# Optimization experiments

Hardware: AMD Instinct MI355X
Metric: run time of the kernel (lower is better)

Reference implementation:

```python
import jax, jax.numpy as jnp
import numpy as np

N_NODES = 100000
HID = 32
NUM_FEAT = 64
DAMPING = 0.1
RK4_STEPS = 8


def layer_norm(x, g, b, eps=1e-5):
    m = jnp.mean(x, axis=-1, keepdims=True)
    v = jnp.mean((x - m) ** 2, axis=-1, keepdims=True)
    return (x - m) * jax.lax.rsqrt(v + eps) * g + b


def gcn_conv(x, src, dst, w, b, n):
    # PyG GCNConv: symmetric norm with self-loops (weight 1).
    xw = x @ w                                            # [N,H]
    deg = jax.ops.segment_sum(jnp.ones_like(src, dtype=x.dtype), dst,
                              num_segments=n) + 1.0       # in-degree + self-loop
    dinv = jax.lax.rsqrt(deg)                             # deg^{-1/2}
    coef = (dinv[src] * dinv[dst])[:, None]               # [E,1]
    agg = jax.ops.segment_sum(xw[src] * coef, dst, num_segments=n)
    self_term = xw * (1.0 / deg)[:, None]                 # self-loop: dinv[i]^2
    return agg + self_term + b


def setup_inputs() -> dict:
    key = jax.random.key(0)
    ks = jax.random.split(key, 12)
    x = jax.random.normal(ks[0], (N_NODES, NUM_FEAT), dtype=jnp.float32)
    edge_index_pos = jax.random.randint(ks[1], (2, 1600000), 0, N_NODES, dtype=jnp.int64)
    edge_index_neg = jax.random.randint(ks[2], (2, 1600000), 0, N_NODES, dtype=jnp.int64)
    t = jnp.arange(2, dtype=jnp.float32)
    s = 0.05
    return {
        "x": x,
        "edge_index_pos": edge_index_pos,
        "edge_index_neg": edge_index_neg,
        "t": t,
        "w_enc": jax.random.normal(ks[3], (NUM_FEAT, HID), jnp.float32) * s,
        "b_enc": jnp.zeros((HID,), jnp.float32),
        "g_feat": jnp.ones((HID,), jnp.float32),
        "b_feat": jnp.zeros((HID,), jnp.float32),
        "w_pos": jax.random.normal(ks[4], (HID, HID), jnp.float32) * s,
        "b_pos": jnp.zeros((HID,), jnp.float32),
        "w_neg": jax.random.normal(ks[5], (HID, HID), jnp.float32) * s,
        "b_neg": jnp.zeros((HID,), jnp.float32),
        "w_psi": jax.random.normal(ks[6], (2 * HID, HID), jnp.float32) * s,
        "g_ode": jnp.ones((HID,), jnp.float32),
        "b_ode": jnp.zeros((HID,), jnp.float32),
    }


def reference(x, edge_index_pos, edge_index_neg, t, w_enc, b_enc, g_feat, b_feat,
              w_pos, b_pos, w_neg, b_neg, w_psi, g_ode, b_ode):
    n = x.shape[0]
    src_p, dst_p = edge_index_pos[0], edge_index_pos[1]
    src_n, dst_n = edge_index_neg[0], edge_index_neg[1]

    h0 = layer_norm(x @ w_enc + b_enc, g_feat, b_feat)

    def ode_func(h):
        hn = layer_norm(h, g_ode, b_ode)
        hp = gcn_conv(hn, src_p, dst_p, w_pos, b_pos, n)
        hm = gcn_conv(hn, src_n, dst_n, w_neg, b_neg, n)
        delta = jnp.tanh(jnp.concatenate([hp, hm], axis=1) @ w_psi)  # psi, bias=False
        return jnp.clip(delta - DAMPING * hn, -50.0, 50.0)

    dt = (t[1] - t[0]) / RK4_STEPS  # fixed-step RK4 stand-in for dopri5

    def step(h, _):
        k1 = ode_func(h)
        k2 = ode_func(h + 0.5 * dt * k1)
        k3 = ode_func(h + 0.5 * dt * k2)
        k4 = ode_func(h + dt * k3)
        return h + (dt / 6.0) * (k1 + 2.0 * k2 + 2.0 * k3 + k4), None

    h, _ = jax.lax.scan(step, h0, None, length=RK4_STEPS)
    return h
```

## Files before the change

### kernel.cpp

```cpp
#include <hip/hip_runtime.h>

#define HID 32
#define NFEAT 64


__global__ void hist_kernel(const int* __restrict__ dstP, const int* __restrict__ dstN,
                            int* __restrict__ cntP, int* __restrict__ cntN, int E) {
    int stride = gridDim.x * blockDim.x;
    for (int idx = blockIdx.x * blockDim.x + threadIdx.x; idx < 2 * E; idx += stride) {
        if (idx < E) atomicAdd(&cntP[dstP[idx]], 1);
        else         atomicAdd(&cntN[dstN[idx - E]], 1);
    }
}

__global__ void deg_kernel(const int* __restrict__ cntP, const int* __restrict__ cntN,
                           float* __restrict__ dinvP, float* __restrict__ invdegP,
                           float* __restrict__ dinvN, float* __restrict__ invdegN, int n) {
    int i = blockIdx.x * blockDim.x + threadIdx.x;
    if (i >= n) return;
    float dp = (float)cntP[i] + 1.0f;
    dinvP[i] = rsqrtf(dp);
    invdegP[i] = 1.0f / dp;
    float dn = (float)cntN[i] + 1.0f;
    dinvN[i] = rsqrtf(dn);
    invdegN[i] = 1.0f / dn;
}

__global__ void scan_kernel(const int* __restrict__ cntP, const int* __restrict__ cntN,
                            int* __restrict__ rpP, int* __restrict__ rpN,
                            int* __restrict__ curP, int* __restrict__ curN, int n) {
    const int* cnt = blockIdx.x ? cntN : cntP;
    int* rp  = blockIdx.x ? rpN  : rpP;
    int* cur = blockIdx.x ? curN : curP;
    __shared__ int buf[1024];
    __shared__ int carry;
    int tid = threadIdx.x;
    if (tid == 0) carry = 0;
    __syncthreads();
    for (int base = 0; base < n; base += 1024) {
        int i = base + tid;
        int v = (i < n) ? cnt[i] : 0;
        buf[tid] = v;
        __syncthreads();
        for (int off = 1; off < 1024; off <<= 1) {
            int t = (tid >= off) ? buf[tid - off] : 0;
            __syncthreads();
            buf[tid] += t;
            __syncthreads();
        }
        int c = carry;
        if (i < n) {
            int ex = c + buf[tid] - v;
            rp[i]  = ex;
            cur[i] = ex;
        }
        __syncthreads();
        if (tid == 1023) carry = c + buf[1023];
        __syncthreads();
    }
    if (tid == 0) rp[n] = carry;
}

__global__ void fill_kernel(const int* __restrict__ srcP, const int* __restrict__ dstP,
                            const int* __restrict__ srcN, const int* __restrict__ dstN,
                            const float* __restrict__ dinvP, const float* __restrict__ dinvN,
                            int* __restrict__ curP, int* __restrict__ curN,
                            int2* __restrict__ edP, int2* __restrict__ edN, int E) {
    int stride = gridDim.x * blockDim.x;
    for (int idx = blockIdx.x * blockDim.x + threadIdx.x; idx < 2 * E; idx += stride) {
        if (idx < E) {
            int s = srcP[idx], d = dstP[idx];
            int p = atomicAdd(&curP[d], 1);
            edP[p] = make_int2(s, __float_as_int(dinvP[s] * dinvP[d]));
        } else {
            int e = idx - E;
            int s = srcN[e], d = dstN[e];
            int p = atomicAdd(&curN[d], 1);
            edN[p] = make_int2(s, __float_as_int(dinvN[s] * dinvN[d]));
        }
    }
}


__global__ void wcomb_kernel(const float* __restrict__ wp, const float* __restrict__ bp,
                             const float* __restrict__ wn, const float* __restrict__ bn,
                             const float* __restrict__ psi,
                             float* __restrict__ wpp, float* __restrict__ wnn,
                             float* __restrict__ cb) {
    int tid = threadIdx.x;
    int j = tid >> 5, f = tid & 31;
    float sp = 0.f, sn = 0.f;
    #pragma unroll
    for (int k = 0; k < HID; ++k) {
        sp += wp[j * HID + k] * psi[k * HID + f];
        sn += wn[j * HID + k] * psi[(HID + k) * HID + f];
    }
    wpp[j * HID + f] = sp;
    wnn[j * HID + f] = sn;
    if (j == 0) {
        float s = 0.f;
        #pragma unroll
        for (int k = 0; k < HID; ++k)
            s += bp[k] * psi[k * HID + f] + bn[k] * psi[(HID + k) * HID + f];
        cb[f] = s;
    }
}


__global__ __launch_bounds__(256) void encoder_kernel(
        const float* __restrict__ x, const float* __restrict__ w_enc,
        const float* __restrict__ b_enc, const float* __restrict__ g_feat,
        const float* __restrict__ b_feat, const float* __restrict__ g_ode,
        const float* __restrict__ b_ode,
        float* __restrict__ h, float* __restrict__ hn, int n) {
    __shared__ float sW[NFEAT][HID];
    __shared__ float sBe[HID], sGf[HID], sBf[HID], sGo[HID], sBo[HID];
    for (int k = threadIdx.x; k < NFEAT * HID; k += blockDim.x)
        sW[k >> 5][k & 31] = w_enc[k];
    if (threadIdx.x < HID) {
        sBe[threadIdx.x] = b_enc[threadIdx.x];
        sGf[threadIdx.x] = g_feat[threadIdx.x];
        sBf[threadIdx.x] = b_feat[threadIdx.x];
        sGo[threadIdx.x] = g_ode[threadIdx.x];
        sBo[threadIdx.x] = b_ode[threadIdx.x];
    }
    __syncthreads();
    int i = blockIdx.x * blockDim.x + threadIdx.x;
    if (i >= n) return;

    float acc[HID];
    #pragma unroll
    for (int f = 0; f < HID; ++f) acc[f] = sBe[f];
    const float4* xr = reinterpret_cast<const float4*>(x + (size_t)i * NFEAT);
    #pragma unroll 2
    for (int q = 0; q < NFEAT / 4; ++q) {
        float4 a = xr[q];
        #pragma unroll
        for (int r = 0; r < 4; ++r) {
            float av = (r == 0) ? a.x : (r == 1) ? a.y : (r == 2) ? a.z : a.w;
            const float4* wr = reinterpret_cast<const float4*>(sW[4 * q + r]);
            #pragma unroll
            for (int f4 = 0; f4 < HID / 4; ++f4) {
                float4 w = wr[f4];
                acc[4 * f4 + 0] += av * w.x;
                acc[4 * f4 + 1] += av * w.y;
                acc[4 * f4 + 2] += av * w.z;
                acc[4 * f4 + 3] += av * w.w;
            }
        }
    }
    float m = 0.f;
    #pragma unroll
    for (int f = 0; f < HID; ++f) m += acc[f];
    m *= (1.0f / HID);
    float var = 0.f;
    #pragma unroll
    for (int f = 0; f < HID; ++f) { float d = acc[f] - m; var += d * d; }
    var *= (1.0f / HID);
    float rs = rsqrtf(var + 1e-5f);
    #pragma unroll
    for (int f = 0; f < HID; ++f) acc[f] = (acc[f] - m) * rs * sGf[f] + sBf[f];

    float4* hw = reinterpret_cast<float4*>(h + (size_t)i * HID);
    #pragma unroll
    for (int q = 0; q < HID / 4; ++q)
        hw[q] = make_float4(acc[4*q], acc[4*q+1], acc[4*q+2], acc[4*q+3]);

    m = 0.f;
    #pragma unroll
    for (int f = 0; f < HID; ++f) m += acc[f];
    m *= (1.0f / HID);
    var = 0.f;
    #pragma unroll
    for (int f = 0; f < HID; ++f) { float d = acc[f] - m; var += d * d; }
    var *= (1.0f / HID);
    rs = rsqrtf(var + 1e-5f);
    float4* hnw = reinterpret_cast<float4*>(hn + (size_t)i * HID);
    #pragma unroll
    for (int q = 0; q < HID / 4; ++q)
        hnw[q] = make_float4((acc[4*q+0] - m) * rs * sGo[4*q+0] + sBo[4*q+0],
                             (acc[4*q+1] - m) * rs * sGo[4*q+1] + sBo[4*q+1],
                             (acc[4*q+2] - m) * rs * sGo[4*q+2] + sBo[4*q+2],
                             (acc[4*q+3] - m) * rs * sGo[4*q+3] + sBo[4*q+3]);
}


template<int STAGE, bool LAST>
__global__ __launch_bounds__(256) void fused_kernel(
        const float* __restrict__ hn_cur, float* __restrict__ hn_next,
        const int* __restrict__ rpP, const int2* __restrict__ edP,
        const float* __restrict__ invdegP,
        const int* __restrict__ rpN, const int2* __restrict__ edN,
        const float* __restrict__ invdegN,
        const float* __restrict__ wpp, const float* __restrict__ wnn,
        const float* __restrict__ cb,
        const float* __restrict__ g_ode, const float* __restrict__ b_ode,
        const float* __restrict__ t,
        float* __restrict__ h, float* __restrict__ kacc,
        float* __restrict__ out, int n) {
    __shared__ float sWp[HID][HID];
    __shared__ float sWn[HID][HID];
    __shared__ float sCb[HID], sGo[HID], sBo[HID];
    for (int k = threadIdx.x; k < HID * HID; k += blockDim.x) {
        sWp[k >> 5][k & 31] = wpp[k];
        sWn[k >> 5][k & 31] = wnn[k];
    }
    if (threadIdx.x < HID) {
        sCb[threadIdx.x] = cb[threadIdx.x];
        sGo[threadIdx.x] = g_ode[threadIdx.x];
        sBo[threadIdx.x] = b_ode[threadIdx.x];
    }
    __syncthreads();

    int g = (blockIdx.x * blockDim.x + threadIdx.x) >> 5;
    int f = threadIdx.x & 31;
    if (g >= n) return;
    size_t base = (size_t)g * HID;
    float hn_self = hn_cur[base + f];

    float accp = invdegP[g] * hn_self;
    {
        int e = rpP[g];
        const int end = rpP[g + 1];
        float a0 = 0.f, a1 = 0.f, a2 = 0.f, a3 = 0.f;
        float a4 = 0.f, a5 = 0.f, a6 = 0.f, a7 = 0.f;
        for (; e + 8 <= end; e += 8) {
            int2 m0 = edP[e+0]; int2 m1 = edP[e+1]; int2 m2 = edP[e+2]; int2 m3 = edP[e+3];
            int2 m4 = edP[e+4]; int2 m5 = edP[e+5]; int2 m6 = edP[e+6]; int2 m7 = edP[e+7];
            a0 += __int_as_float(m0.y) * hn_cur[(size_t)m0.x * HID + f];
            a1 += __int_as_float(m1.y) * hn_cur[(size_t)m1.x * HID + f];
            a2 += __int_as_float(m2.y) * hn_cur[(size_t)m2.x * HID + f];
            a3 += __int_as_float(m3.y) * hn_cur[(size_t)m3.x * HID + f];
            a4 += __int_as_float(m4.y) * hn_cur[(size_t)m4.x * HID + f];
            a5 += __int_as_float(m5.y) * hn_cur[(size_t)m5.x * HID + f];
            a6 += __int_as_float(m6.y) * hn_cur[(size_t)m6.x * HID + f];
            a7 += __int_as_float(m7.y) * hn_cur[(size_t)m7.x * HID + f];
        }
        if (e + 4 <= end) {
            int2 m0 = edP[e+0]; int2 m1 = edP[e+1]; int2 m2 = edP[e+2]; int2 m3 = edP[e+3];
            a0 += __int_as_float(m0.y) * hn_cur[(size_t)m0.x * HID + f];
            a1 += __int_as_float(m1.y) * hn_cur[(size_t)m1.x * HID + f];
            a2 += __int_as_float(m2.y) * hn_cur[(size_t)m2.x * HID + f];
            a3 += __int_as_float(m3.y) * hn_cur[(size_t)m3.x * HID + f];
            e += 4;
        }
        for (; e < end; ++e) {
            int2 m = edP[e];
            a0 += __int_as_float(m.y) * hn_cur[(size_t)m.x * HID + f];
        }
        accp += ((a0 + a1) + (a2 + a3)) + ((a4 + a5) + (a6 + a7));
    }
    float accn = invdegN[g] * hn_self;
    {
        int e = rpN[g];
        const int end = rpN[g + 1];
        float a0 = 0.f, a1 = 0.f, a2 = 0.f, a3 = 0.f;
        float a4 = 0.f, a5 = 0.f, a6 = 0.f, a7 = 0.f;
        for (; e + 8 <= end; e += 8) {
            int2 m0 = edN[e+0]; int2 m1 = edN[e+1]; int2 m2 = edN[e+2]; int2 m3 = edN[e+3];
            int2 m4 = edN[e+4]; int2 m5 = edN[e+5]; int2 m6 = edN[e+6]; int2 m7 = edN[e+7];
            a0 += __int_as_float(m0.y) * hn_cur[(size_t)m0.x * HID + f];
            a1 += __int_as_float(m1.y) * hn_cur[(size_t)m1.x * HID + f];
            a2 += __int_as_float(m2.y) * hn_cur[(size_t)m2.x * HID + f];
            a3 += __int_as_float(m3.y) * hn_cur[(size_t)m3.x * HID + f];
            a4 += __int_as_float(m4.y) * hn_cur[(size_t)m4.x * HID + f];
            a5 += __int_as_float(m5.y) * hn_cur[(size_t)m5.x * HID + f];
            a6 += __int_as_float(m6.y) * hn_cur[(size_t)m6.x * HID + f];
            a7 += __int_as_float(m7.y) * hn_cur[(size_t)m7.x * HID + f];
        }
        if (e + 4 <= end) {
            int2 m0 = edN[e+0]; int2 m1 = edN[e+1]; int2 m2 = edN[e+2]; int2 m3 = edN[e+3];
            a0 += __int_as_float(m0.y) * hn_cur[(size_t)m0.x * HID + f];
            a1 += __int_as_float(m1.y) * hn_cur[(size_t)m1.x * HID + f];
            a2 += __int_as_float(m2.y) * hn_cur[(size_t)m2.x * HID + f];
            a3 += __int_as_float(m3.y) * hn_cur[(size_t)m3.x * HID + f];
            e += 4;
        }
        for (; e < end; ++e) {
            int2 m = edN[e];
            a0 += __int_as_float(m.y) * hn_cur[(size_t)m.x * HID + f];
        }
        accn += ((a0 + a1) + (a2 + a3)) + ((a4 + a5) + (a6 + a7));
    }

    float val = sCb[f];
    #pragma unroll
    for (int k = 0; k < HID; ++k) {
        float apk = __shfl(accp, k, 32);
        float ank = __shfl(accn, k, 32);
        val += apk * sWp[k][f] + ank * sWn[k][f];
    }

    float kv = tanhf(val) - 0.1f * hn_self;
    kv = fminf(fmaxf(kv, -50.0f), 50.0f);

    const float dt = (t[1] - t[0]) * 0.125f;
    float hb = h[base + f];
    float hnext;
    if (STAGE == 0) {
        kacc[base + f] = kv;
        hnext = hb + 0.5f * dt * kv;
    } else if (STAGE == 1) {
        kacc[base + f] += 2.0f * kv;
        hnext = hb + 0.5f * dt * kv;
    } else if (STAGE == 2) {
        kacc[base + f] += 2.0f * kv;
        hnext = hb + dt * kv;
    } else {
        float ka = kacc[base + f];
        float hnew = hb + (dt * (1.0f / 6.0f)) * (ka + kv);
        if (LAST) {
            out[base + f] = hnew;
            return;
        }
        h[base + f] = hnew;
        hnext = hnew;
    }

    float m = hnext;
    #pragma unroll
    for (int off = 16; off > 0; off >>= 1) m += __shfl_xor(m, off, 32);
    m *= (1.0f / HID);
    float d = hnext - m;
    float v2 = d * d;
    #pragma unroll
    for (int off = 16; off > 0; off >>= 1) v2 += __shfl_xor(v2, off, 32);
    float rs = rsqrtf(v2 * (1.0f / HID) + 1e-5f);
    hn_next[base + f] = d * rs * sGo[f] + sBo[f];
}


extern "C" void kernel_launch(void* const* d_in, const int* in_sizes, int n_in,
                              void* d_out, int out_size, void* d_ws, size_t ws_size,
                              hipStream_t stream) {
    const float* x      = (const float*)d_in[0];
    const int*   eip    = (const int*)d_in[1];
    const int*   ein    = (const int*)d_in[2];
    const float* t      = (const float*)d_in[3];
    const float* w_enc  = (const float*)d_in[4];
    const float* b_enc  = (const float*)d_in[5];
    const float* g_feat = (const float*)d_in[6];
    const float* b_feat = (const float*)d_in[7];
    const float* w_pos  = (const float*)d_in[8];
    const float* b_pos  = (const float*)d_in[9];
    const float* w_neg  = (const float*)d_in[10];
    const float* b_neg  = (const float*)d_in[11];
    const float* w_psi  = (const float*)d_in[12];
    const float* g_ode  = (const float*)d_in[13];
    const float* b_ode  = (const float*)d_in[14];

    const int n = in_sizes[0] / NFEAT;
    const int E = in_sizes[1] / 2;

    char* p = (char*)d_ws;
    auto carve = [&](size_t bytes) {
        void* r = (void*)p;
        p += (bytes + 255) & ~(size_t)255;
        return r;
    };
    float* h       = (float*)carve((size_t)n * HID * 4);
    float* hnA     = (float*)carve((size_t)n * HID * 4);
    float* hnB     = (float*)carve((size_t)n * HID * 4);
    float* kacc    = (float*)carve((size_t)n * HID * 4);
    float* dinvP   = (float*)carve((size_t)n * 4);
    float* invdegP = (float*)carve((size_t)n * 4);
    float* dinvN   = (float*)carve((size_t)n * 4);
    float* invdegN = (float*)carve((size_t)n * 4);
    int*   cntP    = (int*)carve((size_t)n * 4);
    int*   cntN    = (int*)carve((size_t)n * 4);
    int*   rpP     = (int*)carve((size_t)(n + 1) * 4);
    int*   rpN     = (int*)carve((size_t)(n + 1) * 4);
    int*   curP    = (int*)carve((size_t)n * 4);
    int*   curN    = (int*)carve((size_t)n * 4);
    int2*  edP     = (int2*)carve((size_t)E * 8);
    int2*  edN     = (int2*)carve((size_t)E * 8);
    float* wpp     = (float*)carve((size_t)HID * HID * 4);
    float* wnn     = (float*)carve((size_t)HID * HID * 4);
    float* cbias   = (float*)carve((size_t)HID * 4);
    (void)ws_size; (void)n_in; (void)out_size;

    const int* srcP = eip;
    const int* dstP = eip + E;
    const int* srcN = ein;
    const int* dstN = ein + E;

    hipMemsetAsync(cntP, 0, (size_t)n * 4, stream);
    hipMemsetAsync(cntN, 0, (size_t)n * 4, stream);
    hist_kernel<<<2048, 256, 0, stream>>>(dstP, dstN, cntP, cntN, E);
    deg_kernel<<<(n + 255) / 256, 256, 0, stream>>>(cntP, cntN, dinvP, invdegP, dinvN, invdegN, n);
    scan_kernel<<<2, 1024, 0, stream>>>(cntP, cntN, rpP, rpN, curP, curN, n);
    fill_kernel<<<2048, 256, 0, stream>>>(srcP, dstP, srcN, dstN, dinvP, dinvN,
                                          curP, curN, edP, edN, E);
    wcomb_kernel<<<1, 1024, 0, stream>>>(w_pos, b_pos, w_neg, b_neg, w_psi, wpp, wnn, cbias);

    encoder_kernel<<<(n + 255) / 256, 256, 0, stream>>>(x, w_enc, b_enc, g_feat, b_feat,
                                                        g_ode, b_ode, h, hnA, n);

    const int fg = (n * HID + 255) / 256;
    float* cur = hnA;
    float* nxt = hnB;
    for (int s = 0; s < 8; ++s) {
        for (int st = 0; st < 4; ++st) {
            bool last = (s == 7 && st == 3);
            if (st == 0)
                fused_kernel<0, false><<<fg, 256, 0, stream>>>(cur, nxt, rpP, edP, invdegP,
                    rpN, edN, invdegN, wpp, wnn, cbias, g_ode, b_ode, t, h, kacc,
                    (float*)d_out, n);
            else if (st == 1)
                fused_kernel<1, false><<<fg, 256, 0, stream>>>(cur, nxt, rpP, edP, invdegP,
                    rpN, edN, invdegN, wpp, wnn, cbias, g_ode, b_ode, t, h, kacc,
                    (float*)d_out, n);
            else if (st == 2)
                fused_kernel<2, false><<<fg, 256, 0, stream>>>(cur, nxt, rpP, edP, invdegP,
                    rpN, edN, invdegN, wpp, wnn, cbias, g_ode, b_ode, t, h, kacc,
                    (float*)d_out, n);
            else if (!last)
                fused_kernel<3, false><<<fg, 256, 0, stream>>>(cur, nxt, rpP, edP, invdegP,
                    rpN, edN, invdegN, wpp, wnn, cbias, g_ode, b_ode, t, h, kacc,
                    (float*)d_out, n);
            else
                fused_kernel<3, true><<<fg, 256, 0, stream>>>(cur, nxt, rpP, edP, invdegP,
                    rpN, edN, invdegN, wpp, wnn, cbias, g_ode, b_ode, t, h, kacc,
                    (float*)d_out, n);
            float* tmp = cur; cur = nxt; nxt = tmp;
        }
    }
}
```

Before: 3.897 ms.

## Store normalized hidden state in fp16 and parallelize CSR prefix scan

The layer-normed state gathered by the 32 fused ODE-stage kernels is now stored as half precision instead of fp32. This halves the bytes of every random neighbour gather and of the per-stage write. Separately, the single-block serial prefix scan is replaced by a three-kernel block-parallel scan (local scan, partial-sum scan, offset add). The fp16 storage adds rounding error to the activations, and the new scan costs extra kernel launches.

```diff
diff --git a/kernel.cpp b/kernel.cpp
--- a/kernel.cpp
+++ b/kernel.cpp
@@ -1,4 +1,5 @@
 #include <hip/hip_runtime.h>
+#include <hip/hip_fp16.h>
 
 #define HID 32
 #define NFEAT 64
@@ -26,39 +27,88 @@
     invdegN[i] = 1.0f / dn;
 }
 
-__global__ void scan_kernel(const int* __restrict__ cntP, const int* __restrict__ cntN,
-                            int* __restrict__ rpP, int* __restrict__ rpN,
-                            int* __restrict__ curP, int* __restrict__ curN, int n) {
-    const int* cnt = blockIdx.x ? cntN : cntP;
-    int* rp  = blockIdx.x ? rpN  : rpP;
-    int* cur = blockIdx.x ? curN : curP;
-    __shared__ int buf[1024];
-    __shared__ int carry;
+
+__global__ __launch_bounds__(256) void scanA_kernel(
+        const int* __restrict__ cntP, const int* __restrict__ cntN,
+        int* __restrict__ rpP, int* __restrict__ rpN,
+        int* __restrict__ partials, int n, int nb) {
+    int gb = blockIdx.x;
+    int graph = (gb >= nb) ? 1 : 0;
+    int b = graph ? gb - nb : gb;
+    const int* cnt = graph ? cntN : cntP;
+    int* rp = graph ? rpN : rpP;
+    __shared__ int tsum[256];
     int tid = threadIdx.x;
-    if (tid == 0) carry = 0;
+    int base = b * 1024 + tid * 4;
+    int v[4];
+    int s = 0;
+    #pragma unroll
+    for (int k = 0; k < 4; ++k) {
+        int i = base + k;
+        v[k] = (i < n) ? cnt[i] : 0;
+        s += v[k];
+    }
+    tsum[tid] = s;
     __syncthreads();
-    for (int base = 0; base < n; base += 1024) {
-        int i = base + tid;
-        int v = (i < n) ? cnt[i] : 0;
-        buf[tid] = v;
+    for (int off = 1; off < 256; off <<= 1) {
+        int t = (tid >= off) ? tsum[tid - off] : 0;
         __syncthreads();
-        for (int off = 1; off < 1024; off <<= 1) {
-            int t = (tid >= off) ? buf[tid - off] : 0;
-            __syncthreads();
-            buf[tid] += t;
-            __syncthreads();
-        }
-        int c = carry;
+        tsum[tid] += t;
+        __syncthreads();
+    }
+    int ex = tsum[tid] - s;
+    #pragma unroll
+    for (int k = 0; k < 4; ++k) {
+        int i = base + k;
+        if (i < n) rp[i] = ex;
+        ex += v[k];
+    }
+    if (tid == 255) partials[gb] = tsum[255];
+}
+
+__global__ __launch_bounds__(256) void scanB_kernel(
+        int* __restrict__ partials, int* __restrict__ rpP, int* __restrict__ rpN,
+        int n, int nb) {
+    int graph = blockIdx.x;
+    int* part = partials + graph * nb;
+    __shared__ int buf[256];
+    int tid = threadIdx.x;
+    int v = (tid < nb) ? part[tid] : 0;
+    buf[tid] = v;
+    __syncthreads();
+    for (int off = 1; off < 256; off <<= 1) {
+        int t = (tid >= off) ? buf[tid - off] : 0;
+        __syncthreads();
+        buf[tid] += t;
+        __syncthreads();
+    }
+    if (tid < nb) part[tid] = buf[tid] - v;
+    if (tid == 255) {
+        int* rp = graph ? rpN : rpP;
+        rp[n] = buf[255];
+    }
+}
+
+__global__ __launch_bounds__(256) void scanC_kernel(
+        int* __restrict__ rpP, int* __restrict__ rpN,
+        int* __restrict__ curP, int* __restrict__ curN,
+        const int* __restrict__ partials, int n, int nb) {
+    int gb = blockIdx.x;
+    int graph = (gb >= nb) ? 1 : 0;
+    int b = graph ? gb - nb : gb;
+    int* rp  = graph ? rpN  : rpP;
+    int* cur = graph ? curN : curP;
+    int off = partials[gb];
+    int base = b * 1024 + threadIdx.x * 4;
+    #pragma unroll
+    for (int k = 0; k < 4; ++k) {
+        int i = base + k;
         if (i < n) {
-            int ex = c + buf[tid] - v;
-            rp[i]  = ex;
-            cur[i] = ex;
-        }
-        __syncthreads();
-        if (tid == 1023) carry = c + buf[1023];
-        __syncthreads();
-    }
-    if (tid == 0) rp[n] = carry;
+            int val = rp[i] + off;
+            rp[i]  = val;
+            cur[i] = val;
+        }
+    }
 }
 
 __global__ void fill_kernel(const int* __restrict__ srcP, const int* __restrict__ dstP,
@@ -112,7 +162,7 @@
         const float* __restrict__ b_enc, const float* __restrict__ g_feat,
         const float* __restrict__ b_feat, const float* __restrict__ g_ode,
         const float* __restrict__ b_ode,
-        float* __restrict__ h, float* __restrict__ hn, int n) {
+        float* __restrict__ h, __half* __restrict__ hn, int n) {
     __shared__ float sW[NFEAT][HID];
     __shared__ float sBe[HID], sGf[HID], sBf[HID], sGo[HID], sBo[HID];
     for (int k = threadIdx.x; k < NFEAT * HID; k += blockDim.x)
@@ -175,19 +225,19 @@
     for (int f = 0; f < HID; ++f) { float d = acc[f] - m; var += d * d; }
     var *= (1.0f / HID);
     rs = rsqrtf(var + 1e-5f);
-    float4* hnw = reinterpret_cast<float4*>(hn + (size_t)i * HID);
-    #pragma unroll
-    for (int q = 0; q < HID / 4; ++q)
-        hnw[q] = make_float4((acc[4*q+0] - m) * rs * sGo[4*q+0] + sBo[4*q+0],
-                             (acc[4*q+1] - m) * rs * sGo[4*q+1] + sBo[4*q+1],
-                             (acc[4*q+2] - m) * rs * sGo[4*q+2] + sBo[4*q+2],
-                             (acc[4*q+3] - m) * rs * sGo[4*q+3] + sBo[4*q+3]);
+    __half2* hnw = reinterpret_cast<__half2*>(hn + (size_t)i * HID);
+    #pragma unroll
+    for (int q = 0; q < HID / 2; ++q) {
+        float v0 = (acc[2*q+0] - m) * rs * sGo[2*q+0] + sBo[2*q+0];
+        float v1 = (acc[2*q+1] - m) * rs * sGo[2*q+1] + sBo[2*q+1];
+        hnw[q] = __floats2half2_rn(v0, v1);
+    }
 }
 
 
 template<int STAGE, bool LAST>
 __global__ __launch_bounds__(256) void fused_kernel(
-        const float* __restrict__ hn_cur, float* __restrict__ hn_next,
+        const __half* __restrict__ hn_cur, __half* __restrict__ hn_next,
         const int* __restrict__ rpP, const int2* __restrict__ edP,
         const float* __restrict__ invdegP,
         const int* __restrict__ rpN, const int2* __restrict__ edN,
@@ -216,7 +266,7 @@
     int f = threadIdx.x & 31;
     if (g >= n) return;
     size_t base = (size_t)g * HID;
-    float hn_self = hn_cur[base + f];
+    float hn_self = __half2float(hn_cur[base + f]);
 
     float accp = invdegP[g] * hn_self;
     {
@@ -227,26 +277,26 @@
         for (; e + 8 <= end; e += 8) {
             int2 m0 = edP[e+0]; int2 m1 = edP[e+1]; int2 m2 = edP[e+2]; int2 m3 = edP[e+3];
             int2 m4 = edP[e+4]; int2 m5 = edP[e+5]; int2 m6 = edP[e+6]; int2 m7 = edP[e+7];
-            a0 += __int_as_float(m0.y) * hn_cur[(size_t)m0.x * HID + f];
-            a1 += __int_as_float(m1.y) * hn_cur[(size_t)m1.x * HID + f];
-            a2 += __int_as_float(m2.y) * hn_cur[(size_t)m2.x * HID + f];
-            a3 += __int_as_float(m3.y) * hn_cur[(size_t)m3.x * HID + f];
-            a4 += __int_as_float(m4.y) * hn_cur[(size_t)m4.x * HID + f];
-            a5 += __int_as_float(m5.y) * hn_cur[(size_t)m5.x * HID + f];
-            a6 += __int_as_float(m6.y) * hn_cur[(size_t)m6.x * HID + f];
-            a7 += __int_as_float(m7.y) * hn_cur[(size_t)m7.x * HID + f];
+            a0 += __int_as_float(m0.y) * __half2float(hn_cur[(size_t)m0.x * HID + f]);
+            a1 += __int_as_float(m1.y) * __half2float(hn_cur[(size_t)m1.x * HID + f]);
+            a2 += __int_as_float(m2.y) * __half2float(hn_cur[(size_t)m2.x * HID + f]);
+            a3 += __int_as_float(m3.y) * __half2float(hn_cur[(size_t)m3.x * HID + f]);
+            a4 += __int_as_float(m4.y) * __half2float(hn_cur[(size_t)m4.x * HID + f]);
+            a5 += __int_as_float(m5.y) * __half2float(hn_cur[(size_t)m5.x * HID + f]);
+            a6 += __int_as_float(m6.y) * __half2float(hn_cur[(size_t)m6.x * HID + f]);
+            a7 += __int_as_float(m7.y) * __half2float(hn_cur[(size_t)m7.x * HID + f]);
         }
         if (e + 4 <= end) {
             int2 m0 = edP[e+0]; int2 m1 = edP[e+1]; int2 m2 = edP[e+2]; int2 m3 = edP[e+3];
-            a0 += __int_as_float(m0.y) * hn_cur[(size_t)m0.x * HID + f];
-            a1 += __int_as_float(m1.y) * hn_cur[(size_t)m1.x * HID + f];
-            a2 += __int_as_float(m2.y) * hn_cur[(size_t)m2.x * HID + f];
-            a3 += __int_as_float(m3.y) * hn_cur[(size_t)m3.x * HID + f];
+            a0 += __int_as_float(m0.y) * __half2float(hn_cur[(size_t)m0.x * HID + f]);
+            a1 += __int_as_float(m1.y) * __half2float(hn_cur[(size_t)m1.x * HID + f]);
+            a2 += __int_as_float(m2.y) * __half2float(hn_cur[(size_t)m2.x * HID + f]);
+            a3 += __int_as_float(m3.y) * __half2float(hn_cur[(size_t)m3.x * HID + f]);
             e += 4;
         }
         for (; e < end; ++e) {
             int2 m = edP[e];
-            a0 += __int_as_float(m.y) * hn_cur[(size_t)m.x * HID + f];
+            a0 += __int_as_float(m.y) * __half2float(hn_cur[(size_t)m.x * HID + f]);
         }
         accp += ((a0 + a1) + (a2 + a3)) + ((a4 + a5) + (a6 + a7));
     }
@@ -259,26 +309,26 @@
         for (; e + 8 <= end; e += 8) {
             int2 m0 = edN[e+0]; int2 m1 = edN[e+1]; int2 m2 = edN[e+2]; int2 m3 = edN[e+3];
             int2 m4 = edN[e+4]; int2 m5 = edN[e+5]; int2 m6 = edN[e+6]; int2 m7 = edN[e+7];
-            a0 += __int_as_float(m0.y) * hn_cur[(size_t)m0.x * HID + f];
-            a1 += __int_as_float(m1.y) * hn_cur[(size_t)m1.x * HID + f];
-            a2 += __int_as_float(m2.y) * hn_cur[(size_t)m2.x * HID + f];
-            a3 += __int_as_float(m3.y) * hn_cur[(size_t)m3.x * HID + f];
-            a4 += __int_as_float(m4.y) * hn_cur[(size_t)m4.x * HID + f];
-            a5 += __int_as_float(m5.y) * hn_cur[(size_t)m5.x * HID + f];
-            a6 += __int_as_float(m6.y) * hn_cur[(size_t)m6.x * HID + f];
-            a7 += __int_as_float(m7.y) * hn_cur[(size_t)m7.x * HID + f];
+            a0 += __int_as_float(m0.y) * __half2float(hn_cur[(size_t)m0.x * HID + f]);
+            a1 += __int_as_float(m1.y) * __half2float(hn_cur[(size_t)m1.x * HID + f]);
+            a2 += __int_as_float(m2.y) * __half2float(hn_cur[(size_t)m2.x * HID + f]);
+            a3 += __int_as_float(m3.y) * __half2float(hn_cur[(size_t)m3.x * HID + f]);
+            a4 += __int_as_float(m4.y) * __half2float(hn_cur[(size_t)m4.x * HID + f]);
+            a5 += __int_as_float(m5.y) * __half2float(hn_cur[(size_t)m5.x * HID + f]);
+            a6 += __int_as_float(m6.y) * __half2float(hn_cur[(size_t)m6.x * HID + f]);
+            a7 += __int_as_float(m7.y) * __half2float(hn_cur[(size_t)m7.x * HID + f]);
         }
         if (e + 4 <= end) {
             int2 m0 = edN[e+0]; int2 m1 = edN[e+1]; int2 m2 = edN[e+2]; int2 m3 = edN[e+3];
-            a0 += __int_as_float(m0.y) * hn_cur[(size_t)m0.x * HID + f];
-            a1 += __int_as_float(m1.y) * hn_cur[(size_t)m1.x * HID + f];
-            a2 += __int_as_float(m2.y) * hn_cur[(size_t)m2.x * HID + f];
-            a3 += __int_as_float(m3.y) * hn_cur[(size_t)m3.x * HID + f];
+            a0 += __int_as_float(m0.y) * __half2float(hn_cur[(size_t)m0.x * HID + f]);
+            a1 += __int_as_float(m1.y) * __half2float(hn_cur[(size_t)m1.x * HID + f]);
+            a2 += __int_as_float(m2.y) * __half2float(hn_cur[(size_t)m2.x * HID + f]);
+            a3 += __int_as_float(m3.y) * __half2float(hn_cur[(size_t)m3.x * HID + f]);
             e += 4;
         }
         for (; e < end; ++e) {
             int2 m = edN[e];
-            a0 += __int_as_float(m.y) * hn_cur[(size_t)m.x * HID + f];
+            a0 += __int_as_float(m.y) * __half2float(hn_cur[(size_t)m.x * HID + f]);
         }
         accn += ((a0 + a1) + (a2 + a3)) + ((a4 + a5) + (a6 + a7));
     }
@@ -326,7 +376,7 @@
     #pragma unroll
     for (int off = 16; off > 0; off >>= 1) v2 += __shfl_xor(v2, off, 32);
     float rs = rsqrtf(v2 * (1.0f / HID) + 1e-5f);
-    hn_next[base + f] = d * rs * sGo[f] + sBo[f];
+    hn_next[base + f] = __float2half(d * rs * sGo[f] + sBo[f]);
 }
 
 
@@ -358,25 +408,27 @@
         p += (bytes + 255) & ~(size_t)255;
         return r;
     };
-    float* h       = (float*)carve((size_t)n * HID * 4);
-    float* hnA     = (float*)carve((size_t)n * HID * 4);
-    float* hnB     = (float*)carve((size_t)n * HID * 4);
-    float* kacc    = (float*)carve((size_t)n * HID * 4);
-    float* dinvP   = (float*)carve((size_t)n * 4);
-    float* invdegP = (float*)carve((size_t)n * 4);
-    float* dinvN   = (float*)carve((size_t)n * 4);
-    float* invdegN = (float*)carve((size_t)n * 4);
-    int*   cntP    = (int*)carve((size_t)n * 4);
-    int*   cntN    = (int*)carve((size_t)n * 4);
-    int*   rpP     = (int*)carve((size_t)(n + 1) * 4);
-    int*   rpN     = (int*)carve((size_t)(n + 1) * 4);
-    int*   curP    = (int*)carve((size_t)n * 4);
-    int*   curN    = (int*)carve((size_t)n * 4);
-    int2*  edP     = (int2*)carve((size_t)E * 8);
-    int2*  edN     = (int2*)carve((size_t)E * 8);
-    float* wpp     = (float*)carve((size_t)HID * HID * 4);
-    float* wnn     = (float*)carve((size_t)HID * HID * 4);
-    float* cbias   = (float*)carve((size_t)HID * 4);
+    float*  h       = (float*)carve((size_t)n * HID * 4);
+    __half* hnA     = (__half*)carve((size_t)n * HID * 2);
+    __half* hnB     = (__half*)carve((size_t)n * HID * 2);
+    float*  kacc    = (float*)carve((size_t)n * HID * 4);
+    float*  dinvP   = (float*)carve((size_t)n * 4);
+    float*  invdegP = (float*)carve((size_t)n * 4);
+    float*  dinvN   = (float*)carve((size_t)n * 4);
+    float*  invdegN = (float*)carve((size_t)n * 4);
+    int*    cntP    = (int*)carve((size_t)n * 4);
+    int*    cntN    = (int*)carve((size_t)n * 4);
+    int*    rpP     = (int*)carve((size_t)(n + 1) * 4);
+    int*    rpN     = (int*)carve((size_t)(n + 1) * 4);
+    int*    curP    = (int*)carve((size_t)n * 4);
+    int*    curN    = (int*)carve((size_t)n * 4);
+    int2*   edP     = (int2*)carve((size_t)E * 8);
+    int2*   edN     = (int2*)carve((size_t)E * 8);
+    float*  wpp     = (float*)carve((size_t)HID * HID * 4);
+    float*  wnn     = (float*)carve((size_t)HID * HID * 4);
+    float*  cbias   = (float*)carve((size_t)HID * 4);
+    const int nb    = (n + 1023) / 1024;
+    int*    partials= (int*)carve((size_t)(2 * nb) * 4);
     (void)ws_size; (void)n_in; (void)out_size;
 
     const int* srcP = eip;
@@ -388,7 +440,9 @@
     hipMemsetAsync(cntN, 0, (size_t)n * 4, stream);
     hist_kernel<<<2048, 256, 0, stream>>>(dstP, dstN, cntP, cntN, E);
     deg_kernel<<<(n + 255) / 256, 256, 0, stream>>>(cntP, cntN, dinvP, invdegP, dinvN, invdegN, n);
-    scan_kernel<<<2, 1024, 0, stream>>>(cntP, cntN, rpP, rpN, curP, curN, n);
+    scanA_kernel<<<2 * nb, 256, 0, stream>>>(cntP, cntN, rpP, rpN, partials, n, nb);
+    scanB_kernel<<<2, 256, 0, stream>>>(partials, rpP, rpN, n, nb);
+    scanC_kernel<<<2 * nb, 256, 0, stream>>>(rpP, rpN, curP, curN, partials, n, nb);
     fill_kernel<<<2048, 256, 0, stream>>>(srcP, dstP, srcN, dstN, dinvP, dinvN,
                                           curP, curN, edP, edN, E);
     wcomb_kernel<<<1, 1024, 0, stream>>>(w_pos, b_pos, w_neg, b_neg, w_psi, wpp, wnn, cbias);
@@ -397,8 +451,8 @@
                                                         g_ode, b_ode, h, hnA, n);
 
     const int fg = (n * HID + 255) / 256;
-    float* cur = hnA;
-    float* nxt = hnB;
+    __half* cur = hnA;
+    __half* nxt = hnB;
     for (int s = 0; s < 8; ++s) {
         for (int st = 0; st < 4; ++st) {
             bool last = (s == 7 && st == 3);
@@ -422,7 +476,7 @@
                 fused_kernel<3, true><<<fg, 256, 0, stream>>>(cur, nxt, rpP, edP, invdegP,
                     rpN, edN, invdegN, wpp, wnn, cbias, g_ode, b_ode, t, h, kacc,
                     (float*)d_out, n);
-            float* tmp = cur; cur = nxt; nxt = tmp;
-        }
-    }
-}
+            __half* tmp = cur; cur = nxt; nxt = tmp;
+        }
+    }
+}
```

Result: faster. 3.686 ms (-5.4%).
